# Kernel optimization log

Measured on AMD Instinct MI355X. Metric: run time of the kernel, lower is better.

Reference implementation:

```python
import jax, jax.numpy as jnp
import numpy as np

L_BBOX, L_GIOU, L_OBJ, AUX_W = 5.0, 2.0, 1.0, 0.5
EPS = 1e-7


def _xyxy(b):
    # cxcywh -> xyxy
    return jnp.concatenate([b[..., :2] - b[..., 2:] * 0.5,
                            b[..., :2] + b[..., 2:] * 0.5], axis=-1)


def _giou(a, b):
    # a, b: [..., 4] xyxy (broadcastable) -> giou [...]
    area_a = (a[..., 2] - a[..., 0]) * (a[..., 3] - a[..., 1])
    area_b = (b[..., 2] - b[..., 0]) * (b[..., 3] - b[..., 1])
    lt = jnp.maximum(a[..., :2], b[..., :2])
    rb = jnp.minimum(a[..., 2:], b[..., 2:])
    wh = jnp.maximum(rb - lt, 0.0)
    inter = wh[..., 0] * wh[..., 1]
    union = area_a + area_b - inter
    iou = inter / (union + EPS)
    lte = jnp.minimum(a[..., :2], b[..., :2])
    rbe = jnp.maximum(a[..., 2:], b[..., 2:])
    whe = jnp.maximum(rbe - lte, 0.0)
    enc = whe[..., 0] * whe[..., 1]
    return iou - (enc - union) / (enc + EPS)


def _bce_sum(logits, targets):
    # numerically stable BCE-with-logits, reduction='sum'
    return jnp.sum(jnp.maximum(logits, 0.0) - logits * targets
                   + jnp.log1p(jnp.exp(-jnp.abs(logits))))


def _hungarian(cost):
    # exact Kuhn-Munkres (shortest augmenting path), rectangular, minimization
    cost = np.asarray(cost, dtype=np.float64)
    transposed = cost.shape[0] > cost.shape[1]
    if transposed:
        cost = cost.T
    n, m = cost.shape
    u = np.zeros(n + 1)
    v = np.zeros(m + 1)
    p = np.zeros(m + 1, dtype=np.int64)
    way = np.zeros(m + 1, dtype=np.int64)
    for i in range(1, n + 1):
        p[0] = i
        j0 = 0
        minv = np.full(m + 1, np.inf)
        used = np.zeros(m + 1, dtype=bool)
        while True:
            used[j0] = True
            i0 = p[j0]
            cur = cost[i0 - 1] - u[i0] - v[1:]
            free = ~used[1:]
            better = free & (cur < minv[1:])
            minv[1:] = np.where(better, cur, minv[1:])
            way[1:] = np.where(better, j0, way[1:])
            free_idx = np.nonzero(free)[0]
            jbest = free_idx[np.argmin(minv[1:][free_idx])]
            delta = minv[1 + jbest]
            u[p[used]] += delta
            v[used] -= delta
            minv[~used] -= delta
            j0 = jbest + 1
            if p[j0] == 0:
                break
        while j0:
            j1 = way[j0]
            p[j0] = p[j1]
            j0 = j1
    rows = p[1:] - 1
    cols = np.nonzero(rows >= 0)[0]
    rows = rows[cols]
    if transposed:
        rows, cols = cols, rows
    return rows.astype(np.int64), cols.astype(np.int64)


def _match(pred_bboxes, target_bboxes, bbox_mask):
    # batched cost matrix built on-device, Hungarian per sample (no_grad path)
    pxy = _xyxy(pred_bboxes)
    txy = _xyxy(target_bboxes)
    c_l1 = jnp.sum(jnp.abs(pred_bboxes[:, :, None, :] - target_bboxes[:, None, :, :]), -1)
    c_giou = -_giou(pxy[:, :, None, :], txy[:, None, :, :])
    C = np.asarray(L_BBOX * c_l1 + L_GIOU * c_giou)        # [B,N,M]
    mask = np.asarray(bbox_mask)
    B, N, M = C.shape
    pidx = np.zeros((B, M), np.int32)
    tidx = np.zeros((B, M), np.int32)
    pm = np.zeros((B, M), np.float32)
    for i in range(B):
        vid = np.nonzero(mask[i] > 0.5)[0]
        k = vid.size
        if k == 0:
            continue
        r, c = _hungarian(C[i][:, vid])
        pidx[i, :k] = r
        tidx[i, :k] = vid[c]
        pm[i, :k] = 1.0
    return jnp.asarray(pidx), jnp.asarray(tidx), jnp.asarray(pm)


def _det_losses(pred_bboxes, obj_logits, target_bboxes, pidx, tidx, pm):
    B, N = pred_bboxes.shape[:2]
    bi = jnp.arange(B)[:, None]
    mp = pred_bboxes[bi, pidx]               # [B,M,4] matched preds (padded)
    mt = target_bboxes[bi, tidx]             # [B,M,4] matched targets
    nb = jnp.maximum(pm.sum(), 1.0)
    bbox_loss = (jnp.abs(mp - mt).sum(-1) * pm).sum() / nb
    giou_loss = ((1.0 - _giou(_xyxy(mp), _xyxy(mt))) * pm).sum() / nb
    obj_t = jnp.zeros((B, N), pred_bboxes.dtype).at[bi, pidx].max(pm)
    obj_loss = _bce_sum(obj_logits[..., 0], obj_t) / (B * N)
    return bbox_loss, giou_loss, obj_loss, obj_t


def _total(cls_logits, label, pred_bboxes, obj_scores, target_bboxes,
           aux_pred_bboxes, aux_obj_scores, pidx, tidx, pm):
    B = cls_logits.shape[0]
    cls_loss = -jax.nn.log_softmax(cls_logits, -1)[jnp.arange(B), label].mean()
    bbox_loss, giou_loss, obj_loss, obj_t = _det_losses(
        pred_bboxes, obj_scores, target_bboxes, pidx, tidx, pm)
    # aux losses, vectorized over L decoder layers
    L = aux_pred_bboxes.shape[0]
    bi = jnp.arange(B)[:, None]
    mpa = aux_pred_bboxes[:, bi, pidx]                      # [L,B,M,4]
    mt = target_bboxes[bi, tidx][None]                      # [1,B,M,4]
    nb = jnp.maximum(pm.sum(), 1.0)
    aux_bbox = (jnp.abs(mpa - mt).sum(-1) * pm[None]).sum() / nb
    aux_giou = ((1.0 - _giou(_xyxy(mpa), _xyxy(mt))) * pm[None]).sum() / nb
    N = pred_bboxes.shape[1]
    aux_obj = _bce_sum(aux_obj_scores[..., 0], obj_t[None]) / (B * N)
    aux_loss = (L_BBOX * aux_bbox + L_GIOU * aux_giou + L_OBJ * aux_obj) * AUX_W / L
    return (cls_loss + L_BBOX * bbox_loss + L_GIOU * giou_loss
            + L_OBJ * obj_loss + aux_loss)


def setup_inputs() -> dict:
    B, N, M, L, C = 32, 300, 60, 5, 1000
    ks = jax.random.split(jax.random.key(0), 9)
    cls_logits = jax.random.normal(ks[0], (B, C), jnp.float32)
    label = jax.random.randint(ks[1], (B,), 0, C)
    pred_bboxes = jax.random.uniform(ks[2], (B, N, 4), jnp.float32)
    obj_scores = jax.random.normal(ks[3], (B, N, 1), jnp.float32)
    cxcy = jax.random.uniform(ks[4], (B, M, 2), jnp.float32, 0.2, 0.8)
    wh = jax.random.uniform(ks[5], (B, M, 2), jnp.float32, 0.05, 0.35)
    target_bboxes = jnp.concatenate([cxcy, wh], -1)
    counts = jax.random.randint(ks[6], (B,), 1, M + 1)
    bbox_mask = (jnp.arange(M)[None, :] < counts[:, None]).astype(jnp.float32)
    aux_pred_bboxes = jax.random.uniform(ks[7], (L, B, N, 4), jnp.float32)
    aux_obj_scores = jax.random.normal(ks[8], (L, B, N, 1), jnp.float32)
    return {"cls_logits": cls_logits, "label": label,
            "pred_bboxes": pred_bboxes, "obj_scores": obj_scores,
            "target_bboxes": target_bboxes, "bbox_mask": bbox_mask,
            "aux_pred_bboxes": aux_pred_bboxes,
            "aux_obj_scores": aux_obj_scores}


def reference(cls_logits, label, pred_bboxes, obj_scores, target_bboxes,
              bbox_mask, aux_pred_bboxes, aux_obj_scores):
    pidx, tidx, pm = _match(pred_bboxes, target_bboxes, bbox_mask)
    return _total(cls_logits, label, pred_bboxes, obj_scores, target_bboxes,
                  aux_pred_bboxes, aux_obj_scores, pidx, tidx, pm)
```

## Files before the change

### kernel.cpp

```cpp
#include <hip/hip_runtime.h>
#include <math.h>

#define BN   32
#define NN   300
#define MM   60
#define LAUX 5
#define CNUM 1000

#define LC_ROWS 53
#define CINF 3.0e38f

#define THR_ROW   1.5f
#define EXB_BATCH 3.0f

#define ACC_CLS   0
#define ACC_OBJ   1
#define ACC_AOBJ  2
#define ACC_BBOX  3
#define ACC_GIOU  4
#define ACC_ABBOX 5
#define ACC_AGIOU 6
#define ACC_NB    7

__device__ float  g_cost[BN * MM * NN + 64];
__device__ int    g_match[BN * NN];
__device__ double g_acc[8];

__device__ __forceinline__ float giou_box(float ax0, float ay0, float ax1, float ay1,
                                          float bx0, float by0, float bx1, float by1) {
    const float EPS = 1e-7f;
    float area_a = (ax1 - ax0) * (ay1 - ay0);
    float area_b = (bx1 - bx0) * (by1 - by0);
    float ltx = fmaxf(ax0, bx0), lty = fmaxf(ay0, by0);
    float rbx = fminf(ax1, bx1), rby = fminf(ay1, by1);
    float w = fmaxf(rbx - ltx, 0.0f), h = fmaxf(rby - lty, 0.0f);
    float inter = w * h;
    float uni = area_a + area_b - inter;
    float iou = inter / (uni + EPS);
    float ex0 = fminf(ax0, bx0), ey0 = fminf(ay0, by0);
    float ex1 = fmaxf(ax1, bx1), ey1 = fmaxf(ay1, by1);
    float ew = fmaxf(ex1 - ex0, 0.0f), eh = fmaxf(ey1 - ey0, 0.0f);
    float enc = ew * eh;
    return iou - (enc - uni) / (enc + EPS);
}

__global__ void cost_kernel(const float* __restrict__ pred, const float* __restrict__ tgt) {
    if (blockIdx.x == 0 && threadIdx.x < 8) g_acc[threadIdx.x] = 0.0;
    int idx = blockIdx.x * blockDim.x + threadIdx.x;
    if (idx >= BN * MM * NN) return;
    int n = idx % NN;
    int m = (idx / NN) % MM;
    int b = idx / (NN * MM);
    const float* p = pred + ((size_t)(b * NN + n)) * 4;
    const float* t = tgt + ((size_t)(b * MM + m)) * 4;
    float p0 = p[0], p1 = p[1], p2 = p[2], p3 = p[3];
    float t0 = t[0], t1 = t[1], t2 = t[2], t3 = t[3];
    float l1 = fabsf(p0 - t0) + fabsf(p1 - t1) + fabsf(p2 - t2) + fabsf(p3 - t3);
    float gi = giou_box(p0 - p2 * 0.5f, p1 - p3 * 0.5f, p0 + p2 * 0.5f, p1 + p3 * 0.5f,
                        t0 - t2 * 0.5f, t1 - t3 * 0.5f, t0 + t2 * 0.5f, t1 + t3 * 0.5f);
    g_cost[idx] = 5.0f * l1 - 2.0f * gi;
}


__device__ __forceinline__ unsigned enc_key(float x, int col) {
    unsigned u = __float_as_uint(x);
    unsigned e = (u & 0x80000000u) ? ~u : (u | 0x80000000u);
    return (e & 0xFFFFFE00u) | (unsigned)col;
}
__device__ __forceinline__ float dec_key(unsigned kk) {
    unsigned e = kk & 0xFFFFFE00u;
    unsigned u = (e & 0x80000000u) ? (e & 0x7FFFFFFFu) : ~e;
    return __uint_as_float(u);
}

__device__ __forceinline__ unsigned wave_min_u32(unsigned k) {
#define WSTEP(C) { unsigned t = (unsigned)__builtin_amdgcn_update_dpp((int)k, (int)k, (C), 0xF, 0xF, false); \
                   k = (t < k) ? t : k; }
    WSTEP(0x111) WSTEP(0x112) WSTEP(0x114) WSTEP(0x118) WSTEP(0x142) WSTEP(0x143)
#undef WSTEP
    return (unsigned)__builtin_amdgcn_readlane((int)k, 63);
}

__device__ __forceinline__ void wave_min_pair(unsigned& a, unsigned& b) {
#define PSTEP(C) { \
    unsigned ta = (unsigned)__builtin_amdgcn_update_dpp((int)a, (int)a, (C), 0xF, 0xF, false); \
    unsigned tb = (unsigned)__builtin_amdgcn_update_dpp((int)b, (int)b, (C), 0xF, 0xF, false); \
    a = (ta < a) ? ta : a; \
    b = (tb < b) ? tb : b; }
    PSTEP(0x111) PSTEP(0x112) PSTEP(0x114) PSTEP(0x118) PSTEP(0x142) PSTEP(0x143)
#undef PSTEP
    a = (unsigned)__builtin_amdgcn_readlane((int)a, 63);
    b = (unsigned)__builtin_amdgcn_readlane((int)b, 63);
}

__device__ __forceinline__ void wave_min2_u32(unsigned& a1, unsigned& a2) {
#define W2STEP(C) { \
    unsigned b1 = (unsigned)__builtin_amdgcn_update_dpp(-1, (int)a1, (C), 0xF, 0xF, false); \
    unsigned b2 = (unsigned)__builtin_amdgcn_update_dpp(-1, (int)a2, (C), 0xF, 0xF, false); \
    unsigned lo = (b1 < a1) ? b1 : a1; \
    unsigned hi = (b1 < a1) ? a1 : b1; \
    unsigned mn = (b2 < a2) ? b2 : a2; \
    a2 = (hi < mn) ? hi : mn; \
    a1 = lo; }
    W2STEP(0x111) W2STEP(0x112) W2STEP(0x114) W2STEP(0x118) W2STEP(0x142) W2STEP(0x143)
#undef W2STEP
    a1 = (unsigned)__builtin_amdgcn_readlane((int)a1, 63);
    a2 = (unsigned)__builtin_amdgcn_readlane((int)a2, 63);
}

__device__ __forceinline__ int sel5i(const int* a, int s) {
    int r = a[0];
    r = (s == 1) ? a[1] : r;
    r = (s == 2) ? a[2] : r;
    r = (s == 3) ? a[3] : r;
    r = (s == 4) ? a[4] : r;
    return r;
}
__device__ __forceinline__ float sel5f(const float* a, int s) {
    float r = a[0];
    r = (s == 1) ? a[1] : r;
    r = (s == 2) ? a[2] : r;
    r = (s == 3) ? a[3] : r;
    r = (s == 4) ? a[4] : r;
    return r;
}
__device__ __forceinline__ int rdlane_i(int x, int l) { return __builtin_amdgcn_readlane(x, l); }
__device__ __forceinline__ float rdlane_f(float x, int l) {
    return __uint_as_float((unsigned)__builtin_amdgcn_readlane(__float_as_int(x), l));
}

__global__ __launch_bounds__(64) void hung_kernel(const float* __restrict__ mask) {
    const int b = blockIdx.x;
    const int lane = threadIdx.x;
    __shared__ __align__(16) float lc[LC_ROWS * NN + 24];
    __shared__ int claimc[NN];

    float mval = (lane < MM) ? mask[b * MM + lane] : 0.0f;
    int k = __popcll(__ballot(mval > 0.5f));

    const float* cb = g_cost + (size_t)b * (MM * NN);
    int stage = (k < LC_ROWS) ? k : LC_ROWS;
    int nf4 = stage * (NN / 4);
    for (int t = lane; t < nf4; t += 64) ((float4*)lc)[t] = ((const float4*)cb)[t];
#pragma unroll
    for (int s = 0; s < 5; s++) {
        int c = s * 64 + lane;
        if (c < NN) claimc[c] = 0x7FFFFFFF;
    }
    __syncthreads();

#define LOAD_ROW(rv, ri) do { int _r = (ri); \
    if (_r < LC_ROWS) { const int _o = _r * NN + lane; \
        rv[0] = lc[_o]; rv[1] = lc[_o + 64]; rv[2] = lc[_o + 128]; \
        rv[3] = lc[_o + 192]; rv[4] = lc[_o + 256]; \
    } else { const float* _g = cb + (size_t)_r * NN + lane; \
        rv[0] = _g[0]; rv[1] = _g[64]; rv[2] = _g[128]; \
        rv[3] = _g[192]; rv[4] = _g[256]; } } while (0)

    float v[5], minv[5], uc[5];
    int pc[5], way[5];
    int used_inv = 0;
#pragma unroll
    for (int s = 0; s < 5; s++) {
        v[s] = 0.0f; uc[s] = 0.0f; pc[s] = 0; way[s] = 0; minv[s] = CINF;
        if (s * 64 + lane >= NN) used_inv |= 1 << s;
    }

    unsigned rowkey = 0xFFFFFFFFu;
    if (lane < k) {
        unsigned best = 0xFFFFFFFFu;
        if (lane < LC_ROWS) {
            const float* rp = lc + lane * NN;
            for (int c = 0; c < NN; c += 4) {
                float4 q = *(const float4*)(rp + c);
                unsigned c0 = enc_key(q.x, c);
                unsigned c1 = enc_key(q.y, c + 1);
                unsigned c2 = enc_key(q.z, c + 2);
                unsigned c3 = enc_key(q.w, c + 3);
                unsigned m01 = (c0 < c1) ? c0 : c1;
                unsigned m23 = (c2 < c3) ? c2 : c3;
                unsigned m = (m01 < m23) ? m01 : m23;
                best = (m < best) ? m : best;
            }
        } else {
            const float* rp = cb + (size_t)lane * NN;
            for (int c = 0; c < NN; c += 4) {
                float4 q = *(const float4*)(rp + c);
                unsigned c0 = enc_key(q.x, c);
                unsigned c1 = enc_key(q.y, c + 1);
                unsigned c2 = enc_key(q.z, c + 2);
                unsigned c3 = enc_key(q.w, c + 3);
                unsigned m01 = (c0 < c1) ? c0 : c1;
                unsigned m23 = (c2 < c3) ? c2 : c3;
                unsigned m = (m01 < m23) ? m01 : m23;
                best = (m < best) ? m : best;
            }
        }
        rowkey = best;
    }
    float u_row = dec_key(rowkey);

    int jr = (int)(rowkey & 0x1FFu);
    if (lane < k) atomicMin(&claimc[jr], (int)lane);
    __syncthreads();
    unsigned long long assigned;
    {
        int jrs = (lane < k) ? jr : 0;
        bool won = (lane < k) && (claimc[jrs] == (int)lane);
        assigned = __ballot(won);
    }
#pragma unroll
    for (int s = 0; s < 5; s++) {
        int c = s * 64 + lane;
        int w = (c < NN) ? claimc[c] : 0x7FFFFFFF;
        bool hit = (w != 0x7FFFFFFF);
        int wm = hit ? w : 0;
        unsigned kw = (unsigned)__builtin_amdgcn_ds_bpermute(wm << 2, (int)rowkey);
        float uw = dec_key(kw);
        pc[s] = hit ? (w + 1) : pc[s];
        uc[s] = hit ? uw : uc[s];
    }

    unsigned long long kmask = (k >= 64) ? ~0ull : ((1ull << k) - 1ull);
    unsigned long long pool = ~assigned & kmask;
    unsigned long long leftover = 0ull;
    {
        unsigned long long once = 0ull, twice = 0ull;
        int guard = 0;
        while (pool && guard++ < 4 * MM + 16) {
            int r = (int)__builtin_ctzll(pool);
            pool &= pool - 1;
            if ((twice >> r) & 1ull) { leftover |= 1ull << r; continue; }
            if ((once >> r) & 1ull) twice |= 1ull << r; else once |= 1ull << r;

            float rv[5];
            LOAD_ROW(rv, r);
            unsigned k1 = 0xFFFFFFFFu, k2 = 0xFFFFFFFFu;
#pragma unroll
            for (int s = 0; s < 5; s++) {
                int c = s * 64 + lane;
                unsigned kk = ((used_inv >> s) & 1) ? 0xFFFFFFFFu : enc_key(rv[s] - v[s], c);
                unsigned lo = (kk < k1) ? kk : k1;
                unsigned hi = (kk < k1) ? k1 : kk;
                k2 = (hi < k2) ? hi : k2;
                k1 = lo;
            }
            wave_min2_u32(k1, k2);
            float m1 = dec_key(k1), m2 = dec_key(k2);
            int j1 = (int)(k1 & 0x1FFu);
            int sl = j1 >> 6, ow = j1 & 63;
            int pj = rdlane_i(sel5i(pc, sl), ow);
            float dv = m2 - m1;
            u_row = (lane == r) ? m2 : u_row;
#pragma unroll
            for (int s = 0; s < 5; s++) {
                bool hit = (lane == ow) && (s == sl);
                v[s]  = hit ? v[s] - dv : v[s];
                pc[s] = hit ? r + 1    : pc[s];
                uc[s] = hit ? m2       : uc[s];
            }
            if (pj > 0) pool |= 1ull << (pj - 1);
        }
        leftover |= pool;
    }

    float exb = EXB_BATCH;
    while (leftover) {
        int r = (int)__builtin_ctzll(leftover);
        leftover &= leftover - 1;

        {
            float rv[5];
            LOAD_ROW(rv, r);
            unsigned kAll = 0xFFFFFFFFu, kFree = 0xFFFFFFFFu;
#pragma unroll
            for (int s = 0; s < 5; s++) {
                int c = s * 64 + lane;
                bool valid = !((used_inv >> s) & 1);
                unsigned kk = valid ? enc_key(rv[s] - v[s], c) : 0xFFFFFFFFu;
                kAll = (kk < kAll) ? kk : kAll;
                unsigned kf = (valid && pc[s] == 0) ? kk : 0xFFFFFFFFu;
                kFree = (kf < kFree) ? kf : kFree;
            }
            wave_min_pair(kAll, kFree);
            float m1 = dec_key(kAll), mf = dec_key(kFree);
            float spend = mf - m1;
            if (spend <= fminf(THR_ROW, exb)) {
                exb -= spend;
                int jf = (int)(kFree & 0x1FFu);
                int slf = jf >> 6, owf = jf & 63;
                u_row = (lane == r) ? m1 : u_row;
#pragma unroll
                for (int s = 0; s < 5; s++) {
                    bool hit = (lane == owf) && (s == slf);
                    pc[s] = hit ? r + 1 : pc[s];
                    uc[s] = hit ? m1    : uc[s];
                }
                continue;
            }
        }

        int used = used_inv;
#pragma unroll
        for (int s = 0; s < 5; s++) minv[s] = CINF;
        float u_cur = rdlane_f(u_row, r);
        float u_i0 = u_cur;
        int i0 = r + 1;
        int j0 = 0;

        for (int guard = 0; guard < NN + 4; guard++) {
            if (j0 > 0) {
                int c0 = j0 - 1, ow0 = c0 & 63, sl0 = c0 >> 6;
                used |= (lane == ow0) ? (1 << sl0) : 0;
            }
            float rv[5];
            LOAD_ROW(rv, i0 - 1);
            unsigned kbest = 0xFFFFFFFFu;
#pragma unroll
            for (int s = 0; s < 5; s++) {
                int c = s * 64 + lane;
                bool skip = (used >> s) & 1;
                float cur = rv[s] - u_i0 - v[s];
                bool lt = !skip && (cur < minv[s]);
                minv[s] = lt ? cur : minv[s];
                way[s]  = lt ? j0 : way[s];
                unsigned kk = skip ? 0xFFFFFFFFu : enc_key(minv[s], c);
                kbest = (kk < kbest) ? kk : kbest;
            }
            unsigned kmin = wave_min_u32(kbest);
            float delta = dec_key(kmin);
            int jb = (int)(kmin & 0x1FFu);

            int sl = jb >> 6, ow = jb & 63;
            int pj = rdlane_i(sel5i(pc, sl), ow);
            float uj = rdlane_f(sel5f(uc, sl), ow);

            u_cur += delta;
#pragma unroll
            for (int s = 0; s < 5; s++) {
                bool us = (used >> s) & 1;
                v[s]    = us ? v[s] - delta   : v[s];
                uc[s]   = us ? uc[s] + delta  : uc[s];
                minv[s] = us ? minv[s]        : minv[s] - delta;
            }

            j0 = jb + 1;
            if (pj == 0) break;
            i0 = pj;
            u_i0 = uj;
        }

        int j = j0;
        int safety = 0;
        while (j && safety++ < NN + 4) {
            int co = j - 1, ow = co & 63, sl = co >> 6;
            int j1 = rdlane_i(sel5i(way, sl), ow);
            int pnew; float unew;
            if (j1 == 0) { pnew = r + 1; unew = u_cur; }
            else {
                int co1 = j1 - 1, ow1 = co1 & 63, sl1 = co1 >> 6;
                pnew = rdlane_i(sel5i(pc, sl1), ow1);
                unew = rdlane_f(sel5f(uc, sl1), ow1);
            }
#pragma unroll
            for (int s = 0; s < 5; s++) {
                bool hit = (lane == ow) && (s == sl);
                pc[s] = hit ? pnew : pc[s];
                uc[s] = hit ? unew : uc[s];
            }
            j = j1;
        }
    }

#pragma unroll
    for (int s = 0; s < 5; s++) {
        int c = s * 64 + lane;
        if (c < NN) g_match[b * NN + c] = pc[s] - 1;
    }
#undef LOAD_ROW
}


__device__ __forceinline__ double bce_term(float x, float t) {
    return (double)(fmaxf(x, 0.0f) - x * t + log1pf(expf(-fabsf(x))));
}

#define PAIR_BLOCKS ((BN * NN + 255) / 256)

__global__ __launch_bounds__(256) void losses_kernel(
    const float* __restrict__ pred, const float* __restrict__ tgt,
    const float* __restrict__ auxp, const float* __restrict__ obj,
    const float* __restrict__ auxobj, const float* __restrict__ logits,
    const int* __restrict__ label)
{
    const int tid = threadIdx.x;
    const int blk = blockIdx.x;
    __shared__ float  smax[256];
    __shared__ double ssum[256];

    if (blk < PAIR_BLOCKS) {
        int idx = blk * 256 + tid;
        double sb = 0.0, sg = 0.0, sab = 0.0, sag = 0.0, nb = 0.0, so = 0.0, sao = 0.0;
        if (idx < BN * NN) {
            int t = g_match[idx];
            float tv = (t >= 0) ? 1.0f : 0.0f;
            so = bce_term(obj[idx], tv);
            for (int l = 0; l < LAUX; l++)
                sao += bce_term(auxobj[l * BN * NN + idx], tv);
            if (t >= 0) {
                int b = idx / NN;
                const float* p = pred + (size_t)idx * 4;
                const float* tg = tgt + ((size_t)(b * MM + t)) * 4;
                float t0 = tg[0], t1 = tg[1], t2 = tg[2], t3 = tg[3];
                float tx0 = t0 - t2 * 0.5f, ty0 = t1 - t3 * 0.5f;
                float tx1 = t0 + t2 * 0.5f, ty1 = t1 + t3 * 0.5f;
                {
                    float p0 = p[0], p1 = p[1], p2 = p[2], p3 = p[3];
                    float l1 = fabsf(p0 - t0) + fabsf(p1 - t1) + fabsf(p2 - t2) + fabsf(p3 - t3);
                    float gi = giou_box(p0 - p2 * 0.5f, p1 - p3 * 0.5f, p0 + p2 * 0.5f, p1 + p3 * 0.5f,
                                        tx0, ty0, tx1, ty1);
                    sb = (double)l1;
                    sg = (double)(1.0f - gi);
                    nb = 1.0;
                }
                for (int l = 0; l < LAUX; l++) {
                    const float* a = auxp + ((size_t)l * BN * NN + idx) * 4;
                    float a0 = a[0], a1 = a[1], a2 = a[2], a3 = a[3];
                    float l1 = fabsf(a0 - t0) + fabsf(a1 - t1) + fabsf(a2 - t2) + fabsf(a3 - t3);
                    float gi = giou_box(a0 - a2 * 0.5f, a1 - a3 * 0.5f, a0 + a2 * 0.5f, a1 + a3 * 0.5f,
                                        tx0, ty0, tx1, ty1);
                    sab += (double)l1;
                    sag += (double)(1.0f - gi);
                }
            }
        }
        for (int off = 32; off; off >>= 1) {
            sb  += __shfl_down(sb, off, 64);
            sg  += __shfl_down(sg, off, 64);
            sab += __shfl_down(sab, off, 64);
            sag += __shfl_down(sag, off, 64);
            nb  += __shfl_down(nb, off, 64);
            so  += __shfl_down(so, off, 64);
            sao += __shfl_down(sao, off, 64);
        }
        if ((tid & 63) == 0) {
            atomicAdd(&g_acc[ACC_BBOX], sb);
            atomicAdd(&g_acc[ACC_GIOU], sg);
            atomicAdd(&g_acc[ACC_ABBOX], sab);
            atomicAdd(&g_acc[ACC_AGIOU], sag);
            atomicAdd(&g_acc[ACC_NB], nb);
            atomicAdd(&g_acc[ACC_OBJ], so);
            atomicAdd(&g_acc[ACC_AOBJ], sao);
        }
    } else {
        const int b = blk - PAIR_BLOCKS;
        const float* row = logits + (size_t)b * CNUM;
        float mx = -1e30f;
        for (int c = tid; c < CNUM; c += 256) mx = fmaxf(mx, row[c]);
        smax[tid] = mx;
        __syncthreads();
        for (int s = 128; s; s >>= 1) {
            if (tid < s) smax[tid] = fmaxf(smax[tid], smax[tid + s]);
            __syncthreads();
        }
        mx = smax[0];
        double s = 0.0;
        for (int c = tid; c < CNUM; c += 256) s += exp((double)(row[c] - mx));
        ssum[tid] = s;
        __syncthreads();
        for (int st = 128; st; st >>= 1) {
            if (tid < st) ssum[tid] += ssum[tid + st];
            __syncthreads();
        }
        if (tid == 0) {
            double lse = log(ssum[0]) + (double)mx;
            atomicAdd(&g_acc[ACC_CLS], lse - (double)row[label[b]]);
        }
    }
}

__global__ void final_kernel(float* __restrict__ out) {
    if (threadIdx.x == 0 && blockIdx.x == 0) {
        double nb = g_acc[ACC_NB];
        if (nb < 1.0) nb = 1.0;
        double cls = g_acc[ACC_CLS] / (double)BN;
        double bbox = g_acc[ACC_BBOX] / nb;
        double giou = g_acc[ACC_GIOU] / nb;
        double obj = g_acc[ACC_OBJ] / (double)(BN * NN);
        double ab = g_acc[ACC_ABBOX] / nb;
        double ag = g_acc[ACC_AGIOU] / nb;
        double ao = g_acc[ACC_AOBJ] / (double)(BN * NN);
        double aux = (5.0 * ab + 2.0 * ag + 1.0 * ao) * 0.5 / (double)LAUX;
        out[0] = (float)(cls + 5.0 * bbox + 2.0 * giou + obj + aux);
    }
}

extern "C" void kernel_launch(void* const* d_in, const int* in_sizes, int n_in,
                              void* d_out, int out_size, void* d_ws, size_t ws_size,
                              hipStream_t stream) {
    const float* cls_logits = (const float*)d_in[0];
    const int* label = (const int*)d_in[1];
    const float* pred_bboxes = (const float*)d_in[2];
    const float* obj_scores = (const float*)d_in[3];
    const float* target_bboxes = (const float*)d_in[4];
    const float* bbox_mask = (const float*)d_in[5];
    const float* aux_pred = (const float*)d_in[6];
    const float* aux_obj = (const float*)d_in[7];
    float* out = (float*)d_out;

    cost_kernel<<<(BN * MM * NN + 255) / 256, 256, 0, stream>>>(pred_bboxes, target_bboxes);
    hung_kernel<<<BN, 64, 0, stream>>>(bbox_mask);
    losses_kernel<<<PAIR_BLOCKS + BN, 256, 0, stream>>>(pred_bboxes, target_bboxes, aux_pred,
                                                        obj_scores, aux_obj, cls_logits, label);
    final_kernel<<<1, 1, 0, stream>>>(out);
}
```

Before: 242.1 us.

## Fuse loss computation into Hungarian kernel and precompute softplus/CE in prep kernel

Removes the separate losses kernel and the g_match buffer. Objectness BCE is split algebraically: the target-independent softplus sum is computed in the cost-building kernel alongside cross-entropy, and the matched -x*t term plus the bbox/GIoU losses are computed directly in the Hungarian kernel epilogue from register-held assignments. Accumulator zeroing moves to the final kernel. This drops one launch and a global round trip for the matching. The risk is that the first call depends on g_acc starting at zero.

```diff
diff --git a/kernel.cpp b/kernel.cpp
--- a/kernel.cpp
+++ b/kernel.cpp
@@ -23,7 +23,6 @@
 #define ACC_NB    7
 
 __device__ float  g_cost[BN * MM * NN + 64];
-__device__ int    g_match[BN * NN];
 __device__ double g_acc[8];
 
 __device__ __forceinline__ float giou_box(float ax0, float ay0, float ax1, float ay1,
@@ -44,21 +43,81 @@
     return iou - (enc - uni) / (enc + EPS);
 }
 
-__global__ void cost_kernel(const float* __restrict__ pred, const float* __restrict__ tgt) {
-    if (blockIdx.x == 0 && threadIdx.x < 8) g_acc[threadIdx.x] = 0.0;
-    int idx = blockIdx.x * blockDim.x + threadIdx.x;
-    if (idx >= BN * MM * NN) return;
-    int n = idx % NN;
-    int m = (idx / NN) % MM;
-    int b = idx / (NN * MM);
-    const float* p = pred + ((size_t)(b * NN + n)) * 4;
-    const float* t = tgt + ((size_t)(b * MM + m)) * 4;
-    float p0 = p[0], p1 = p[1], p2 = p[2], p3 = p[3];
-    float t0 = t[0], t1 = t[1], t2 = t[2], t3 = t[3];
-    float l1 = fabsf(p0 - t0) + fabsf(p1 - t1) + fabsf(p2 - t2) + fabsf(p3 - t3);
-    float gi = giou_box(p0 - p2 * 0.5f, p1 - p3 * 0.5f, p0 + p2 * 0.5f, p1 + p3 * 0.5f,
-                        t0 - t2 * 0.5f, t1 - t3 * 0.5f, t0 + t2 * 0.5f, t1 + t3 * 0.5f);
-    g_cost[idx] = 5.0f * l1 - 2.0f * gi;
+
+#define COST_BLOCKS ((BN * MM * NN + 255) / 256)
+#define SP_ELEMS    (BN * NN * (1 + LAUX))
+#define SP_PER_BLK  2048
+#define SP_BLOCKS   ((SP_ELEMS + SP_PER_BLK - 1) / SP_PER_BLK)
+
+__global__ __launch_bounds__(256) void prep_kernel(
+    const float* __restrict__ pred, const float* __restrict__ tgt,
+    const float* __restrict__ obj, const float* __restrict__ auxobj,
+    const float* __restrict__ logits, const int* __restrict__ label)
+{
+    const int blk = blockIdx.x;
+    const int tid = threadIdx.x;
+    __shared__ float  smax[256];
+    __shared__ double ssum[256];
+
+    if (blk < COST_BLOCKS) {
+        int idx = blk * 256 + tid;
+        if (idx >= BN * MM * NN) return;
+        int n = idx % NN;
+        int m = (idx / NN) % MM;
+        int b = idx / (NN * MM);
+        const float* p = pred + ((size_t)(b * NN + n)) * 4;
+        const float* t = tgt + ((size_t)(b * MM + m)) * 4;
+        float p0 = p[0], p1 = p[1], p2 = p[2], p3 = p[3];
+        float t0 = t[0], t1 = t[1], t2 = t[2], t3 = t[3];
+        float l1 = fabsf(p0 - t0) + fabsf(p1 - t1) + fabsf(p2 - t2) + fabsf(p3 - t3);
+        float gi = giou_box(p0 - p2 * 0.5f, p1 - p3 * 0.5f, p0 + p2 * 0.5f, p1 + p3 * 0.5f,
+                            t0 - t2 * 0.5f, t1 - t3 * 0.5f, t0 + t2 * 0.5f, t1 + t3 * 0.5f);
+        g_cost[idx] = 5.0f * l1 - 2.0f * gi;
+    } else if (blk < COST_BLOCKS + BN) {
+        const int b = blk - COST_BLOCKS;
+        const float* row = logits + (size_t)b * CNUM;
+        float mx = -1e30f;
+        for (int c = tid; c < CNUM; c += 256) mx = fmaxf(mx, row[c]);
+        smax[tid] = mx;
+        __syncthreads();
+        for (int s = 128; s; s >>= 1) {
+            if (tid < s) smax[tid] = fmaxf(smax[tid], smax[tid + s]);
+            __syncthreads();
+        }
+        mx = smax[0];
+        double s = 0.0;
+        for (int c = tid; c < CNUM; c += 256) s += exp((double)(row[c] - mx));
+        ssum[tid] = s;
+        __syncthreads();
+        for (int st = 128; st; st >>= 1) {
+            if (tid < st) ssum[tid] += ssum[tid + st];
+            __syncthreads();
+        }
+        if (tid == 0) {
+            double lse = log(ssum[0]) + (double)mx;
+            atomicAdd(&g_acc[ACC_CLS], lse - (double)row[label[b]]);
+        }
+    } else {
+        int base = (blk - COST_BLOCKS - BN) * SP_PER_BLK;
+        double so = 0.0, sa = 0.0;
+#pragma unroll
+        for (int i = 0; i < SP_PER_BLK / 256; i++) {
+            int e = base + i * 256 + tid;
+            if (e < SP_ELEMS) {
+                float x = (e < BN * NN) ? obj[e] : auxobj[e - BN * NN];
+                double sp = (double)(fmaxf(x, 0.0f) + log1pf(expf(-fabsf(x))));
+                if (e < BN * NN) so += sp; else sa += sp;
+            }
+        }
+        for (int off = 32; off; off >>= 1) {
+            so += __shfl_down(so, off, 64);
+            sa += __shfl_down(sa, off, 64);
+        }
+        if ((tid & 63) == 0) {
+            if (so != 0.0) atomicAdd(&g_acc[ACC_OBJ], so);
+            if (sa != 0.0) atomicAdd(&g_acc[ACC_AOBJ], sa);
+        }
+    }
 }
 
 
@@ -129,7 +188,11 @@
     return __uint_as_float((unsigned)__builtin_amdgcn_readlane(__float_as_int(x), l));
 }
 
-__global__ __launch_bounds__(64) void hung_kernel(const float* __restrict__ mask) {
+__global__ __launch_bounds__(64) void hung_kernel(
+    const float* __restrict__ mask, const float* __restrict__ pred,
+    const float* __restrict__ tgt, const float* __restrict__ obj,
+    const float* __restrict__ auxobj, const float* __restrict__ auxp)
+{
     const int b = blockIdx.x;
     const int lane = threadIdx.x;
     __shared__ __align__(16) float lc[LC_ROWS * NN + 24];
@@ -372,58 +435,32 @@
         }
     }
 
-#pragma unroll
-    for (int s = 0; s < 5; s++) {
-        int c = s * 64 + lane;
-        if (c < NN) g_match[b * NN + c] = pc[s] - 1;
-    }
-#undef LOAD_ROW
-}
-
-
-__device__ __forceinline__ double bce_term(float x, float t) {
-    return (double)(fmaxf(x, 0.0f) - x * t + log1pf(expf(-fabsf(x))));
-}
-
-#define PAIR_BLOCKS ((BN * NN + 255) / 256)
-
-__global__ __launch_bounds__(256) void losses_kernel(
-    const float* __restrict__ pred, const float* __restrict__ tgt,
-    const float* __restrict__ auxp, const float* __restrict__ obj,
-    const float* __restrict__ auxobj, const float* __restrict__ logits,
-    const int* __restrict__ label)
-{
-    const int tid = threadIdx.x;
-    const int blk = blockIdx.x;
-    __shared__ float  smax[256];
-    __shared__ double ssum[256];
-
-    if (blk < PAIR_BLOCKS) {
-        int idx = blk * 256 + tid;
-        double sb = 0.0, sg = 0.0, sab = 0.0, sag = 0.0, nb = 0.0, so = 0.0, sao = 0.0;
-        if (idx < BN * NN) {
-            int t = g_match[idx];
-            float tv = (t >= 0) ? 1.0f : 0.0f;
-            so = bce_term(obj[idx], tv);
-            for (int l = 0; l < LAUX; l++)
-                sao += bce_term(auxobj[l * BN * NN + idx], tv);
-            if (t >= 0) {
-                int b = idx / NN;
-                const float* p = pred + (size_t)idx * 4;
+    {
+        double sb = 0.0, sg = 0.0, sab = 0.0, sag = 0.0, nb = 0.0;
+        double som = 0.0, saom = 0.0;
+#pragma unroll
+        for (int s = 0; s < 5; s++) {
+            int c = s * 64 + lane;
+            int t = pc[s] - 1;
+            if (c < NN && t >= 0) {
+                int idx = b * NN + c;
+                som += (double)obj[idx];
                 const float* tg = tgt + ((size_t)(b * MM + t)) * 4;
                 float t0 = tg[0], t1 = tg[1], t2 = tg[2], t3 = tg[3];
                 float tx0 = t0 - t2 * 0.5f, ty0 = t1 - t3 * 0.5f;
                 float tx1 = t0 + t2 * 0.5f, ty1 = t1 + t3 * 0.5f;
+                const float* p = pred + (size_t)idx * 4;
                 {
                     float p0 = p[0], p1 = p[1], p2 = p[2], p3 = p[3];
                     float l1 = fabsf(p0 - t0) + fabsf(p1 - t1) + fabsf(p2 - t2) + fabsf(p3 - t3);
                     float gi = giou_box(p0 - p2 * 0.5f, p1 - p3 * 0.5f, p0 + p2 * 0.5f, p1 + p3 * 0.5f,
                                         tx0, ty0, tx1, ty1);
-                    sb = (double)l1;
-                    sg = (double)(1.0f - gi);
-                    nb = 1.0;
+                    sb += (double)l1;
+                    sg += (double)(1.0f - gi);
+                    nb += 1.0;
                 }
                 for (int l = 0; l < LAUX; l++) {
+                    saom += (double)auxobj[l * BN * NN + idx];
                     const float* a = auxp + ((size_t)l * BN * NN + idx) * 4;
                     float a0 = a[0], a1 = a[1], a2 = a[2], a3 = a[3];
                     float l1 = fabsf(a0 - t0) + fabsf(a1 - t1) + fabsf(a2 - t2) + fabsf(a3 - t3);
@@ -435,48 +472,25 @@
             }
         }
         for (int off = 32; off; off >>= 1) {
-            sb  += __shfl_down(sb, off, 64);
-            sg  += __shfl_down(sg, off, 64);
-            sab += __shfl_down(sab, off, 64);
-            sag += __shfl_down(sag, off, 64);
-            nb  += __shfl_down(nb, off, 64);
-            so  += __shfl_down(so, off, 64);
-            sao += __shfl_down(sao, off, 64);
-        }
-        if ((tid & 63) == 0) {
+            sb   += __shfl_down(sb, off, 64);
+            sg   += __shfl_down(sg, off, 64);
+            sab  += __shfl_down(sab, off, 64);
+            sag  += __shfl_down(sag, off, 64);
+            nb   += __shfl_down(nb, off, 64);
+            som  += __shfl_down(som, off, 64);
+            saom += __shfl_down(saom, off, 64);
+        }
+        if (lane == 0) {
             atomicAdd(&g_acc[ACC_BBOX], sb);
             atomicAdd(&g_acc[ACC_GIOU], sg);
             atomicAdd(&g_acc[ACC_ABBOX], sab);
             atomicAdd(&g_acc[ACC_AGIOU], sag);
             atomicAdd(&g_acc[ACC_NB], nb);
-            atomicAdd(&g_acc[ACC_OBJ], so);
-            atomicAdd(&g_acc[ACC_AOBJ], sao);
-        }
-    } else {
-        const int b = blk - PAIR_BLOCKS;
-        const float* row = logits + (size_t)b * CNUM;
-        float mx = -1e30f;
-        for (int c = tid; c < CNUM; c += 256) mx = fmaxf(mx, row[c]);
-        smax[tid] = mx;
-        __syncthreads();
-        for (int s = 128; s; s >>= 1) {
-            if (tid < s) smax[tid] = fmaxf(smax[tid], smax[tid + s]);
-            __syncthreads();
-        }
-        mx = smax[0];
-        double s = 0.0;
-        for (int c = tid; c < CNUM; c += 256) s += exp((double)(row[c] - mx));
-        ssum[tid] = s;
-        __syncthreads();
-        for (int st = 128; st; st >>= 1) {
-            if (tid < st) ssum[tid] += ssum[tid + st];
-            __syncthreads();
-        }
-        if (tid == 0) {
-            double lse = log(ssum[0]) + (double)mx;
-            atomicAdd(&g_acc[ACC_CLS], lse - (double)row[label[b]]);
-        }
-    }
+            atomicAdd(&g_acc[ACC_OBJ], -som);
+            atomicAdd(&g_acc[ACC_AOBJ], -saom);
+        }
+    }
+#undef LOAD_ROW
 }
 
 __global__ void final_kernel(float* __restrict__ out) {
@@ -492,6 +506,7 @@
         double ao = g_acc[ACC_AOBJ] / (double)(BN * NN);
         double aux = (5.0 * ab + 2.0 * ag + 1.0 * ao) * 0.5 / (double)LAUX;
         out[0] = (float)(cls + 5.0 * bbox + 2.0 * giou + obj + aux);
+        for (int i = 0; i < 8; i++) g_acc[i] = 0.0;
     }
 }
 
@@ -508,9 +523,9 @@
     const float* aux_obj = (const float*)d_in[7];
     float* out = (float*)d_out;
 
-    cost_kernel<<<(BN * MM * NN + 255) / 256, 256, 0, stream>>>(pred_bboxes, target_bboxes);
-    hung_kernel<<<BN, 64, 0, stream>>>(bbox_mask);
-    losses_kernel<<<PAIR_BLOCKS + BN, 256, 0, stream>>>(pred_bboxes, target_bboxes, aux_pred,
-                                                        obj_scores, aux_obj, cls_logits, label);
+    prep_kernel<<<COST_BLOCKS + BN + SP_BLOCKS, 256, 0, stream>>>(
+        pred_bboxes, target_bboxes, obj_scores, aux_obj, cls_logits, label);
+    hung_kernel<<<BN, 64, 0, stream>>>(bbox_mask, pred_bboxes, target_bboxes,
+                                       obj_scores, aux_obj, aux_pred);
     final_kernel<<<1, 1, 0, stream>>>(out);
 }
```

Result: no change. 243.7 us (+0.7%).
